# Performance work log

Measured on AMD Instinct MI355X. Metric: run time of the kernel, lower is better.

## Reference

```python
import jax, jax.numpy as jnp
import numpy as np
from jax import lax

B, S, D, H, O = 128, 256, 128, 512, 25
TEMP = 0.1


def _init(key, shape, scale):
    return jax.random.uniform(key, shape, jnp.float32, -scale, scale)


def setup_inputs() -> dict:
    key = jax.random.key(0)
    ks = jax.random.split(key, 24)
    sH = 1.0 / np.sqrt(H)
    s2H = 1.0 / np.sqrt(2 * H)
    sD = 1.0 / np.sqrt(D)
    inp = {
        "x": jax.random.normal(ks[0], (B, S, D), jnp.float32),
        "noise_u": jnp.clip(jax.random.uniform(ks[1], (S, B, 1), jnp.float32), 1e-6, 1 - 1e-6),
        # layer_cin: Linear(D, H)
        "w_cin": _init(ks[2], (D, H), sD), "b_cin": _init(ks[3], (H,), sD),
        # layer_c MLP: 2H->2H (x3, ReLU) -> 1
        "w1": _init(ks[4], (2 * H, 2 * H), s2H), "b1": _init(ks[5], (2 * H,), s2H),
        "w2": _init(ks[6], (2 * H, 2 * H), s2H), "b2": _init(ks[7], (2 * H,), s2H),
        "w3": _init(ks[8], (2 * H, 2 * H), s2H), "b3": _init(ks[9], (2 * H,), s2H),
        "w4": _init(ks[10], (2 * H, 1), s2H), "b4": _init(ks[11], (1,), s2H),
        # GRUCell(H, H): gates ordered (r, z, n)
        "w_ih": _init(ks[12], (H, 3 * H), sH), "b_ih": _init(ks[13], (3 * H,), sH),
        "w_hh": _init(ks[14], (H, 3 * H), sH), "b_hh": _init(ks[15], (3 * H,), sH),
        # output Linear(H, O)
        "w_out": _init(ks[16], (H, O), sH), "b_out": _init(ks[17], (O,), sH),
    }
    return inp


def _gru_cell(x, h, w_ih, b_ih, w_hh, b_hh):
    gx = x @ w_ih + b_ih  # [B, 3H]
    gh = h @ w_hh + b_hh
    xr, xz, xn = jnp.split(gx, 3, axis=-1)
    hr, hz, hn = jnp.split(gh, 3, axis=-1)
    r = jax.nn.sigmoid(xr + hr)
    z = jax.nn.sigmoid(xz + hz)
    n = jnp.tanh(xn + r * hn)
    return (1.0 - z) * n + z * h


def reference(x, noise_u, w_cin, b_cin, w1, b1, w2, b2, w3, b3, w4, b4,
              w_ih, b_ih, w_hh, b_hh, w_out, b_out):
    xs = jnp.transpose(x, (1, 0, 2))  # [S, B, D]

    def step(carry, inp):
        c, h, n = carry
        x_t, u = inp
        c_in = jnp.tanh(x_t @ w_cin + b_cin)  # [B, H]
        com = jnp.concatenate([c, c_in], axis=1)  # [B, 2H]
        z = jax.nn.relu(com @ w1 + b1)
        z = jax.nn.relu(z @ w2 + b2)
        z = jax.nn.relu(z @ w3 + b3)
        alpha_logit = z @ w4 + b4  # [B, 1]
        # RelaxedBernoulli(temp=0.1).sample(): sigmoid((logits + logistic noise)/T), detached
        logistic = jnp.log(u) - jnp.log1p(-u)
        alpha = lax.stop_gradient(jax.nn.sigmoid((alpha_logit + logistic) / TEMP))
        h_gru = _gru_cell(c, h, w_ih, b_ih, w_hh, b_hh)
        h_new = h * (1.0 - alpha) + alpha * h_gru
        new_n = n * (1.0 - alpha) + 1.0
        c_new = (c * n * (1.0 - alpha) + c_in) / new_n
        return (c_new, h_new, new_n), None

    c0 = jnp.zeros((B, H), x.dtype)
    h0 = jnp.zeros((B, H), x.dtype)
    n0 = jnp.zeros((B, 1), x.dtype)
    (c, h, n), _ = lax.scan(step, (c0, h0, n0), (xs, noise_u))
    h = _gru_cell(c, h, w_ih, b_ih, w_hh, b_hh)  # final post-loop GRU step
    return h @ w_out + b_out
```

## Files before the change

### kernel.cpp

```cpp
#include <hip/hip_runtime.h>
#include <math.h>

#define SLEN 256
#define BSZ  128
#define DIN  128
#define HSZ  512
#define HH2  1024
#define GG3  1536
#define OSZ  25

typedef _Float16 h8 __attribute__((ext_vector_type(8)));
typedef float    f4 __attribute__((ext_vector_type(4)));

struct P_t {
  const float *x, *noise, *b_cin, *b1, *b2, *b3, *w4, *b4, *b_ih, *b_hh, *w_out, *b_out;
  _Float16 *WT1, *WT2, *WT3, *WTih, *WThh, *WTcin;
  _Float16 *FW1, *FW2, *FW3, *FWih, *FWhh;
  _Float16 *CIN, *COMlo, *Z1, *Z2, *HF16;
  float *LOGI, *GX, *GH, *PART, *HF32, *CF32, *NF32;
  float *out;
};

__device__ __forceinline__ f4 mfma16(h8 a, h8 b, f4 c) {
  return __builtin_amdgcn_mfma_f32_16x16x32_f16(a, b, c, 0, 0, 0);
}

__global__ __launch_bounds__(256) void transpose_cvt(const float* __restrict__ src,
    _Float16* __restrict__ dst, int K, int N) {
  __shared__ float tl[32][33];
  int nt = N >> 5;
  int bx = blockIdx.x % nt, by = blockIdx.x / nt;
  int n0 = bx << 5, k0 = by << 5;
  int tx = threadIdx.x & 31, ty = threadIdx.x >> 5;
#pragma unroll
  for (int i = 0; i < 4; ++i) {
    int r = ty + (i << 3);
    tl[r][tx] = src[(size_t)(k0 + r) * N + n0 + tx];
  }
  __syncthreads();
#pragma unroll
  for (int i = 0; i < 4; ++i) {
    int r = ty + (i << 3);
    dst[(size_t)(n0 + r) * K + k0 + tx] = (_Float16)tl[tx][r];
  }
}

__global__ __launch_bounds__(512) void fragpack(const _Float16* __restrict__ src,
    _Float16* __restrict__ dst, int K) {
  int ct = blockIdx.x;
  int chunks = (K / 32) * 64;
  for (int idx = threadIdx.x; idx < chunks; idx += 512) {
    int i = idx >> 6, lane = idx & 63;
    int mlw = lane & 15, qw = lane >> 4;
    *(h8*)(dst + ((size_t)ct * (K / 32) + i) * 512 + (size_t)lane * 8) =
        *(const h8*)(src + ((size_t)ct * 16 + mlw) * K + i * 32 + qw * 8);
  }
}

__global__ __launch_bounds__(256) void cin_kernel(P_t P) {
  int tid = blockIdx.x * blockDim.x + threadIdx.x;
  if (tid < SLEN * BSZ) {
    float u = P.noise[tid];
    P.LOGI[tid] = logf(u) - log1pf(-u);
  }
  int gw = tid >> 6, lane = tid & 63;
  int nw = (gridDim.x * blockDim.x) >> 6;
  int ml = lane & 15, q = lane >> 4;
  const int MT = (SLEN * BSZ) / 16;
  for (int tt = gw; tt < MT * 8; tt += nw) {
    int mt = tt & (MT - 1), nt = tt / MT;
    int m0 = mt * 16, n0 = nt * 64;
    int m = m0 + ml, b = m & 127, s = m >> 7;
    const float* ap = P.x + ((size_t)b * SLEN + s) * DIN + q * 8;
    const _Float16* bp = P.WTcin + (size_t)(n0 + ml) * DIN + q * 8;
    f4 a0 = {0,0,0,0}, a1 = a0, a2 = a0, a3 = a0;
#pragma unroll
    for (int k = 0; k < DIN; k += 32) {
      f4 lo = *(const f4*)(ap + k);
      f4 hi = *(const f4*)(ap + k + 4);
      h8 av;
      av[0] = (_Float16)lo[0]; av[1] = (_Float16)lo[1];
      av[2] = (_Float16)lo[2]; av[3] = (_Float16)lo[3];
      av[4] = (_Float16)hi[0]; av[5] = (_Float16)hi[1];
      av[6] = (_Float16)hi[2]; av[7] = (_Float16)hi[3];
      a0 = mfma16(av, *(const h8*)(bp + k),            a0);
      a1 = mfma16(av, *(const h8*)(bp + 16*DIN + k),   a1);
      a2 = mfma16(av, *(const h8*)(bp + 32*DIN + k),   a2);
      a3 = mfma16(av, *(const h8*)(bp + 48*DIN + k),   a3);
    }
#pragma unroll
    for (int r = 0; r < 4; ++r) {
      int row = m0 + q * 4 + r;
      int c0 = n0 + ml;
      P.CIN[(size_t)row * HSZ + c0     ] = (_Float16)tanhf(a0[r] + P.b_cin[c0]);
      P.CIN[(size_t)row * HSZ + c0 + 16] = (_Float16)tanhf(a1[r] + P.b_cin[c0 + 16]);
      P.CIN[(size_t)row * HSZ + c0 + 32] = (_Float16)tanhf(a2[r] + P.b_cin[c0 + 32]);
      P.CIN[(size_t)row * HSZ + c0 + 48] = (_Float16)tanhf(a3[r] + P.b_cin[c0 + 48]);
    }
  }
}

__global__ __launch_bounds__(256) void init_kernel(P_t P) {
  int idx = blockIdx.x * 256 + threadIdx.x;
  if (idx < BSZ * HSZ) {
    P.HF32[idx] = 0.f; P.CF32[idx] = 0.f;
    P.HF16[idx] = (_Float16)0.f; P.COMlo[idx] = (_Float16)0.f;
  }
  if (idx < BSZ) P.NF32[idx] = 0.f;
}

__global__ __launch_bounds__(256) void step_a(P_t P, int t, int base) {
  const int tid = threadIdx.x;
  const int lane = tid & 63, wv = tid >> 6;
  const int ml = lane & 15, q = lane >> 4;
  const int g = base + blockIdx.x * 4 + wv;
  f4 acc = {0.f, 0.f, 0.f, 0.f};
  if (g < 512) {
    int rt = g & 7, ct = g >> 3;
    int m0 = rt * 16, col = ct * 16 + ml;
    const _Float16* a0 = P.COMlo + (size_t)(m0 + ml) * HSZ + q * 8;
    const _Float16* a1 = P.CIN + ((size_t)t * BSZ + m0 + ml) * HSZ + q * 8;
    const _Float16* bp = P.FW1 + (size_t)ct * 32 * 512 + (size_t)lane * 8;
#pragma unroll
    for (int i = 0; i < 16; ++i)
      acc = mfma16(*(const h8*)(a0 + i * 32), *(const h8*)(bp + (size_t)i * 512), acc);
#pragma unroll
    for (int i = 0; i < 16; ++i)
      acc = mfma16(*(const h8*)(a1 + i * 32), *(const h8*)(bp + (size_t)(16 + i) * 512), acc);
    float bia = P.b1[col];
#pragma unroll
    for (int j = 0; j < 4; ++j)
      P.Z1[(size_t)(m0 + q * 4 + j) * HH2 + col] = (_Float16)fmaxf(acc[j] + bia, 0.f);
  } else if (g < 1280) {
    int u = g - 512, rt = u & 7, ct = u >> 3;
    int m0 = rt * 16, col = ct * 16 + ml;
    const _Float16* a0 = P.COMlo + (size_t)(m0 + ml) * HSZ + q * 8;
    const _Float16* bp = P.FWih + (size_t)ct * 16 * 512 + (size_t)lane * 8;
#pragma unroll
    for (int i = 0; i < 16; ++i)
      acc = mfma16(*(const h8*)(a0 + i * 32), *(const h8*)(bp + (size_t)i * 512), acc);
    float bia = P.b_ih[col];
#pragma unroll
    for (int j = 0; j < 4; ++j)
      P.GX[(size_t)(m0 + q * 4 + j) * GG3 + col] = acc[j] + bia;
  } else {
    int u = g - 1280, rt = u & 7, ct = u >> 3;
    int m0 = rt * 16, col = ct * 16 + ml;
    const _Float16* a0 = P.HF16 + (size_t)(m0 + ml) * HSZ + q * 8;
    const _Float16* bp = P.FWhh + (size_t)ct * 16 * 512 + (size_t)lane * 8;
#pragma unroll
    for (int i = 0; i < 16; ++i)
      acc = mfma16(*(const h8*)(a0 + i * 32), *(const h8*)(bp + (size_t)i * 512), acc);
    float bia = P.b_hh[col];
#pragma unroll
    for (int j = 0; j < 4; ++j)
      P.GH[(size_t)(m0 + q * 4 + j) * GG3 + col] = acc[j] + bia;
  }
}

__global__ __launch_bounds__(256) void step_b(P_t P) {
  const int tid = threadIdx.x;
  const int lane = tid & 63, wv = tid >> 6;
  const int ml = lane & 15, q = lane >> 4;
  const int g = blockIdx.x * 4 + wv;
  int rt = g & 7, ct = g >> 3;
  int m0 = rt * 16, col = ct * 16 + ml;
  const _Float16* a0 = P.Z1 + (size_t)(m0 + ml) * HH2 + q * 8;
  const _Float16* bp = P.FW2 + (size_t)ct * 32 * 512 + (size_t)lane * 8;
  f4 acc = {0.f, 0.f, 0.f, 0.f};
#pragma unroll
  for (int i = 0; i < 32; ++i)
    acc = mfma16(*(const h8*)(a0 + i * 32), *(const h8*)(bp + (size_t)i * 512), acc);
  float bia = P.b2[col];
#pragma unroll
  for (int j = 0; j < 4; ++j)
    P.Z2[(size_t)(m0 + q * 4 + j) * HH2 + col] = (_Float16)fmaxf(acc[j] + bia, 0.f);
}

__global__ __launch_bounds__(256) void step_c(P_t P) {
  const int tid = threadIdx.x;
  const int lane = tid & 63, wv = tid >> 6;
  const int ml = lane & 15, q = lane >> 4;
  const int g = blockIdx.x * 4 + wv;
  int rt = g & 7, ct = g >> 3;
  int m0 = rt * 16, col = ct * 16 + ml;
  const _Float16* a0 = P.Z2 + (size_t)(m0 + ml) * HH2 + q * 8;
  const _Float16* bp = P.FW3 + (size_t)ct * 32 * 512 + (size_t)lane * 8;
  f4 acc = {0.f, 0.f, 0.f, 0.f};
#pragma unroll
  for (int i = 0; i < 32; ++i)
    acc = mfma16(*(const h8*)(a0 + i * 32), *(const h8*)(bp + (size_t)i * 512), acc);
  float bia = P.b3[col], w4v = P.w4[col];
#pragma unroll
  for (int j = 0; j < 4; ++j) {
    float v = fmaxf(acc[j] + bia, 0.f) * w4v;
    v += __shfl_xor(v, 1); v += __shfl_xor(v, 2);
    v += __shfl_xor(v, 4); v += __shfl_xor(v, 8);
    if (ml == 0) P.PART[(size_t)ct * BSZ + m0 + q * 4 + j] = v;
  }
}

__global__ __launch_bounds__(512) void step_d(P_t P, int t) {
  __shared__ float sa[4];
  const int r = blockIdx.x, tid = threadIdx.x;
  if (tid < 64) {
    float v = P.PART[(size_t)tid * BSZ + r];
#pragma unroll
    for (int off = 32; off > 0; off >>= 1) v += __shfl_xor(v, off);
    if (tid == 0) {
      float lg = (v + P.b4[0] + P.LOGI[(size_t)t * BSZ + r]) * 10.0f;
      float alpha = 1.f / (1.f + expf(-lg));
      float om = 1.f - alpha;
      float n_old = P.NF32[r];
      float nnew = n_old * om + 1.f;
      P.NF32[r] = nnew;
      sa[0] = alpha; sa[1] = om; sa[2] = n_old * om; sa[3] = nnew;
    }
  }
  __syncthreads();
  float alpha = sa[0], om = sa[1], nom = sa[2], nnew = sa[3];
  int col = tid;
  size_t go = (size_t)r * GG3 + col;
  float xr = P.GX[go], xz = P.GX[go + 512], xn = P.GX[go + 1024];
  float hr = P.GH[go], hz = P.GH[go + 512], hn = P.GH[go + 1024];
  float rg = 1.f / (1.f + expf(-(xr + hr)));
  float zg = 1.f / (1.f + expf(-(xz + hz)));
  float ng = tanhf(xn + rg * hn);
  size_t ho = (size_t)r * HSZ + col;
  float h_old = P.HF32[ho];
  float hg = (1.f - zg) * ng + zg * h_old;
  float hnew = h_old * om + alpha * hg;
  P.HF32[ho] = hnew; P.HF16[ho] = (_Float16)hnew;
  float c_old = P.CF32[ho];
  float cin_t = (float)P.CIN[((size_t)t * BSZ + r) * HSZ + col];
  float cnew = (c_old * nom + cin_t) / nnew;
  P.CF32[ho] = cnew; P.COMlo[ho] = (_Float16)cnew;
}

__global__ __launch_bounds__(512) void final_kernel(P_t P) {
  __shared__ float hf[512];
  const int r = blockIdx.x, tid = threadIdx.x;
  const int lane = tid & 63, wv = tid >> 6;
  {
    int col = tid;
    size_t go = (size_t)r * GG3 + col;
    float xr = P.GX[go], xz = P.GX[go + 512], xn = P.GX[go + 1024];
    float hr = P.GH[go], hz = P.GH[go + 512], hn = P.GH[go + 1024];
    float rg = 1.f / (1.f + expf(-(xr + hr)));
    float zg = 1.f / (1.f + expf(-(xz + hz)));
    float ng = tanhf(xn + rg * hn);
    float h_old = P.HF32[(size_t)r * HSZ + col];
    hf[col] = (1.f - zg) * ng + zg * h_old;
  }
  __syncthreads();
  for (int c = wv; c < OSZ; c += 8) {
    float v = 0.f;
#pragma unroll
    for (int j = 0; j < 8; ++j)
      v += hf[lane + 64 * j] * P.w_out[(size_t)(lane + 64 * j) * OSZ + c];
#pragma unroll
    for (int off = 32; off > 0; off >>= 1) v += __shfl_xor(v, off);
    if (lane == 0) P.out[r * OSZ + c] = v + P.b_out[c];
  }
}

extern "C" void kernel_launch(void* const* d_in, const int* in_sizes, int n_in,
                              void* d_out, int out_size, void* d_ws, size_t ws_size,
                              hipStream_t stream) {
  const float* x     = (const float*)d_in[0];
  const float* noise = (const float*)d_in[1];
  const float* w_cin = (const float*)d_in[2];
  const float* b_cin = (const float*)d_in[3];
  const float* w1    = (const float*)d_in[4];
  const float* b1    = (const float*)d_in[5];
  const float* w2    = (const float*)d_in[6];
  const float* b2    = (const float*)d_in[7];
  const float* w3    = (const float*)d_in[8];
  const float* b3    = (const float*)d_in[9];
  const float* w4    = (const float*)d_in[10];
  const float* b4    = (const float*)d_in[11];
  const float* w_ih  = (const float*)d_in[12];
  const float* b_ih  = (const float*)d_in[13];
  const float* w_hh  = (const float*)d_in[14];
  const float* b_hh  = (const float*)d_in[15];
  const float* w_out = (const float*)d_in[16];
  const float* b_out = (const float*)d_in[17];

  char* ws = (char*)d_ws;
  size_t off = 0;
  auto alloc = [&](size_t bytes) -> void* {
    void* p = ws + off;
    off = (off + bytes + 255) & ~(size_t)255;
    return p;
  };

  P_t P;
  P.x = x; P.noise = noise; P.b_cin = b_cin; P.b1 = b1; P.b2 = b2; P.b3 = b3;
  P.w4 = w4; P.b4 = b4; P.b_ih = b_ih; P.b_hh = b_hh; P.w_out = w_out; P.b_out = b_out;
  P.WT1   = (_Float16*)alloc((size_t)HH2 * HH2 * 2);
  P.WT2   = (_Float16*)alloc((size_t)HH2 * HH2 * 2);
  P.WT3   = (_Float16*)alloc((size_t)HH2 * HH2 * 2);
  P.WTih  = (_Float16*)alloc((size_t)GG3 * HSZ * 2);
  P.WThh  = (_Float16*)alloc((size_t)GG3 * HSZ * 2);
  P.WTcin = (_Float16*)alloc((size_t)HSZ * DIN * 2);
  P.FW1   = (_Float16*)alloc((size_t)HH2 * HH2 * 2);
  P.FW2   = (_Float16*)alloc((size_t)HH2 * HH2 * 2);
  P.FW3   = (_Float16*)alloc((size_t)HH2 * HH2 * 2);
  P.FWih  = (_Float16*)alloc((size_t)GG3 * HSZ * 2);
  P.FWhh  = (_Float16*)alloc((size_t)GG3 * HSZ * 2);
  P.CIN   = (_Float16*)alloc((size_t)SLEN * BSZ * HSZ * 2);
  P.COMlo = (_Float16*)alloc((size_t)BSZ * HSZ * 2);
  P.Z1    = (_Float16*)alloc((size_t)BSZ * HH2 * 2);
  P.Z2    = (_Float16*)alloc((size_t)BSZ * HH2 * 2);
  P.HF16  = (_Float16*)alloc((size_t)BSZ * HSZ * 2);
  P.LOGI  = (float*)alloc((size_t)SLEN * BSZ * 4);
  P.GX    = (float*)alloc((size_t)BSZ * GG3 * 4);
  P.GH    = (float*)alloc((size_t)BSZ * GG3 * 4);
  P.PART  = (float*)alloc((size_t)64 * BSZ * 4);
  P.HF32  = (float*)alloc((size_t)BSZ * HSZ * 4);
  P.CF32  = (float*)alloc((size_t)BSZ * HSZ * 4);
  P.NF32  = (float*)alloc((size_t)BSZ * 4);
  P.out   = (float*)d_out;

  transpose_cvt<<<(HH2/32)*(HH2/32), 256, 0, stream>>>(w1, P.WT1, HH2, HH2);
  transpose_cvt<<<(HH2/32)*(HH2/32), 256, 0, stream>>>(w2, P.WT2, HH2, HH2);
  transpose_cvt<<<(HH2/32)*(HH2/32), 256, 0, stream>>>(w3, P.WT3, HH2, HH2);
  transpose_cvt<<<(GG3/32)*(HSZ/32), 256, 0, stream>>>(w_ih, P.WTih, HSZ, GG3);
  transpose_cvt<<<(GG3/32)*(HSZ/32), 256, 0, stream>>>(w_hh, P.WThh, HSZ, GG3);
  transpose_cvt<<<(HSZ/32)*(DIN/32), 256, 0, stream>>>(w_cin, P.WTcin, DIN, HSZ);
  fragpack<<<HH2/16, 512, 0, stream>>>(P.WT1, P.FW1, HH2);
  fragpack<<<HH2/16, 512, 0, stream>>>(P.WT2, P.FW2, HH2);
  fragpack<<<HH2/16, 512, 0, stream>>>(P.WT3, P.FW3, HH2);
  fragpack<<<GG3/16, 512, 0, stream>>>(P.WTih, P.FWih, HSZ);
  fragpack<<<GG3/16, 512, 0, stream>>>(P.WThh, P.FWhh, HSZ);

  cin_kernel<<<1024, 256, 0, stream>>>(P);
  init_kernel<<<256, 256, 0, stream>>>(P);

  for (int t = 0; t < SLEN; ++t) {
    step_a<<<512, 256, 0, stream>>>(P, t, 0);
    step_b<<<128, 256, 0, stream>>>(P);
    step_c<<<128, 256, 0, stream>>>(P);
    step_d<<<BSZ, 512, 0, stream>>>(P, t);
  }
  step_a<<<384, 256, 0, stream>>>(P, 0, 512);
  final_kernel<<<BSZ, 512, 0, stream>>>(P);
}
```

Measured before the change: 7.152 ms.

## Fuse per-step state update into GEMM kernels, cutting launches per timestep

The separate step_d kernel goes away. The GRU gate math moves into the third MLP GEMM kernel, which writes HGRU, and the alpha/h/c/n update moves into the prologue of the first GEMM kernel. That kernel recomputes the update redundantly in each block and stages the fp16 c, h and c_in tiles in LDS. State is now double-buffered, and only one block per row tile writes the fp32 state back. This removes one kernel launch and its global round trip per timestep (256 in total), at the cost of redundant elementwise work in every k1 block and extra LDS traffic.

After: 7.037 ms. About the same (-1.6%).

```diff
diff --git a/kernel.cpp b/kernel.cpp
--- a/kernel.cpp
+++ b/kernel.cpp
@@ -10,14 +10,16 @@
 #define OSZ  25
 
 typedef _Float16 h8 __attribute__((ext_vector_type(8)));
+typedef _Float16 h4v __attribute__((ext_vector_type(4)));
 typedef float    f4 __attribute__((ext_vector_type(4)));
 
 struct P_t {
   const float *x, *noise, *b_cin, *b1, *b2, *b3, *w4, *b4, *b_ih, *b_hh, *w_out, *b_out;
   _Float16 *WT1, *WT2, *WT3, *WTih, *WThh, *WTcin;
   _Float16 *FW1, *FW2, *FW3, *FWih, *FWhh;
-  _Float16 *CIN, *COMlo, *Z1, *Z2, *HF16;
-  float *LOGI, *GX, *GH, *PART, *HF32, *CF32, *NF32;
+  _Float16 *CIN, *Z1, *Z2;
+  float *LOGI, *GX, *GH, *PART, *HGRU;
+  float *CF, *HF, *NF;
   float *out;
 };
 
@@ -102,55 +104,132 @@
 
 __global__ __launch_bounds__(256) void init_kernel(P_t P) {
   int idx = blockIdx.x * 256 + threadIdx.x;
-  if (idx < BSZ * HSZ) {
-    P.HF32[idx] = 0.f; P.CF32[idx] = 0.f;
-    P.HF16[idx] = (_Float16)0.f; P.COMlo[idx] = (_Float16)0.f;
-  }
-  if (idx < BSZ) P.NF32[idx] = 0.f;
-}
-
-__global__ __launch_bounds__(256) void step_a(P_t P, int t, int base) {
+  if (idx < 2 * BSZ * HSZ) { P.CF[idx] = 0.f; P.HF[idx] = 0.f; }
+  if (idx < 2 * BSZ) P.NF[idx] = 0.f;
+}
+
+__global__ __launch_bounds__(256) void step_k1(P_t P, int it) {
   const int tid = threadIdx.x;
   const int lane = tid & 63, wv = tid >> 6;
   const int ml = lane & 15, q = lane >> 4;
-  const int g = base + blockIdx.x * 4 + wv;
-  f4 acc = {0.f, 0.f, 0.f, 0.f};
-  if (g < 512) {
-    int rt = g & 7, ct = g >> 3;
-    int m0 = rt * 16, col = ct * 16 + ml;
-    const _Float16* a0 = P.COMlo + (size_t)(m0 + ml) * HSZ + q * 8;
-    const _Float16* a1 = P.CIN + ((size_t)t * BSZ + m0 + ml) * HSZ + q * 8;
-    const _Float16* bp = P.FW1 + (size_t)ct * 32 * 512 + (size_t)lane * 8;
-#pragma unroll
-    for (int i = 0; i < 16; ++i)
-      acc = mfma16(*(const h8*)(a0 + i * 32), *(const h8*)(bp + (size_t)i * 512), acc);
-#pragma unroll
-    for (int i = 0; i < 16; ++i)
-      acc = mfma16(*(const h8*)(a1 + i * 32), *(const h8*)(bp + (size_t)(16 + i) * 512), acc);
-    float bia = P.b1[col];
-#pragma unroll
-    for (int j = 0; j < 4; ++j)
-      P.Z1[(size_t)(m0 + q * 4 + j) * HH2 + col] = (_Float16)fmaxf(acc[j] + bia, 0.f);
-  } else if (g < 1280) {
-    int u = g - 512, rt = u & 7, ct = u >> 3;
-    int m0 = rt * 16, col = ct * 16 + ml;
-    const _Float16* a0 = P.COMlo + (size_t)(m0 + ml) * HSZ + q * 8;
+  const int b = blockIdx.x;
+  const int rt = b >> 6, bu = b & 63;
+  const int m0 = rt << 4;
+
+  __shared__ _Float16 sC[16][520];
+  __shared__ _Float16 sH[16][520];
+  __shared__ _Float16 sCIN[16][520];
+  __shared__ float sAl[16], sNOM[16], sNN[16];
+
+  if (it == 0) {
+    for (int c4 = tid; c4 < 2048; c4 += 256) {
+      int rl = c4 >> 7, cb = (c4 & 127) << 2;
+      h4v z = {(_Float16)0.f, (_Float16)0.f, (_Float16)0.f, (_Float16)0.f};
+      *(h4v*)&sC[rl][cb] = z;
+      *(h4v*)&sH[rl][cb] = z;
+    }
+  } else {
+    const int s = it - 1;
+    const float* CFo = P.CF + (size_t)((s + 1) & 1) * BSZ * HSZ;
+    const float* HFo = P.HF + (size_t)((s + 1) & 1) * BSZ * HSZ;
+    const float* NFo = P.NF + ((s + 1) & 1) * BSZ;
+    float* CFn = P.CF + (size_t)(s & 1) * BSZ * HSZ;
+    float* HFn = P.HF + (size_t)(s & 1) * BSZ * HSZ;
+    float* NFn = P.NF + (s & 1) * BSZ;
+    {
+      int rl = tid >> 4, sg = tid & 15;
+      int row = m0 + rl;
+      float v = P.PART[(size_t)(sg * 4 + 0) * BSZ + row]
+              + P.PART[(size_t)(sg * 4 + 1) * BSZ + row]
+              + P.PART[(size_t)(sg * 4 + 2) * BSZ + row]
+              + P.PART[(size_t)(sg * 4 + 3) * BSZ + row];
+      v += __shfl_xor(v, 1); v += __shfl_xor(v, 2);
+      v += __shfl_xor(v, 4); v += __shfl_xor(v, 8);
+      if (sg == 0) {
+        float lg = (v + P.b4[0] + P.LOGI[(size_t)s * BSZ + row]) * 10.0f;
+        float al = 1.f / (1.f + expf(-lg));
+        float om = 1.f - al;
+        float no = NFo[row];
+        float nn = no * om + 1.f;
+        sAl[rl] = al; sNOM[rl] = no * om; sNN[rl] = nn;
+        if (bu == 0) NFn[row] = nn;
+      }
+    }
+    __syncthreads();
+    for (int c4 = tid; c4 < 2048; c4 += 256) {
+      int rl = c4 >> 7, cb = (c4 & 127) << 2;
+      int row = m0 + rl;
+      size_t go = (size_t)row * HSZ + cb;
+      f4 hg = *(const f4*)(P.HGRU + go);
+      f4 ho = *(const f4*)(HFo + go);
+      f4 co = *(const f4*)(CFo + go);
+      h4v ci = *(const h4v*)(P.CIN + ((size_t)s * BSZ + row) * HSZ + cb);
+      float al = sAl[rl], om = 1.f - al, nom = sNOM[rl], nn = sNN[rl];
+      f4 hn, cn;
+#pragma unroll
+      for (int j = 0; j < 4; ++j) {
+        hn[j] = ho[j] * om + al * hg[j];
+        cn[j] = (co[j] * nom + (float)ci[j]) / nn;
+      }
+      h4v c16, h16;
+#pragma unroll
+      for (int j = 0; j < 4; ++j) { c16[j] = (_Float16)cn[j]; h16[j] = (_Float16)hn[j]; }
+      *(h4v*)&sC[rl][cb] = c16;
+      *(h4v*)&sH[rl][cb] = h16;
+      if (bu == 0) {
+        *(f4*)(CFn + go) = cn;
+        *(f4*)(HFn + go) = hn;
+      }
+    }
+  }
+  if (bu < 16 && it < SLEN) {
+    for (int c8 = tid; c8 < 1024; c8 += 256) {
+      int rl = c8 >> 6, cb = (c8 & 63) << 3;
+      *(h8*)&sCIN[rl][cb] =
+          *(const h8*)(P.CIN + ((size_t)it * BSZ + m0 + rl) * HSZ + cb);
+    }
+  }
+  __syncthreads();
+
+  const int u = bu * 4 + wv;
+  if (u < 64) {
+    if (it < SLEN) {
+      int ct = u, col = (ct << 4) + ml;
+      const _Float16* bp = P.FW1 + (size_t)ct * 32 * 512 + (size_t)lane * 8;
+      const _Float16* ac = &sC[ml][q * 8];
+      const _Float16* ai = &sCIN[ml][q * 8];
+      f4 acc = {0.f, 0.f, 0.f, 0.f};
+#pragma unroll
+      for (int k = 0; k < 16; ++k)
+        acc = mfma16(*(const h8*)(ac + k * 32), *(const h8*)(bp + (size_t)k * 512), acc);
+#pragma unroll
+      for (int k = 0; k < 16; ++k)
+        acc = mfma16(*(const h8*)(ai + k * 32), *(const h8*)(bp + (size_t)(16 + k) * 512), acc);
+      float bia = P.b1[col];
+#pragma unroll
+      for (int j = 0; j < 4; ++j)
+        P.Z1[(size_t)(m0 + q * 4 + j) * HH2 + col] = (_Float16)fmaxf(acc[j] + bia, 0.f);
+    }
+  } else if (u < 160) {
+    int ct = u - 64, col = (ct << 4) + ml;
     const _Float16* bp = P.FWih + (size_t)ct * 16 * 512 + (size_t)lane * 8;
-#pragma unroll
-    for (int i = 0; i < 16; ++i)
-      acc = mfma16(*(const h8*)(a0 + i * 32), *(const h8*)(bp + (size_t)i * 512), acc);
+    const _Float16* a0 = &sC[ml][q * 8];
+    f4 acc = {0.f, 0.f, 0.f, 0.f};
+#pragma unroll
+    for (int k = 0; k < 16; ++k)
+      acc = mfma16(*(const h8*)(a0 + k * 32), *(const h8*)(bp + (size_t)k * 512), acc);
     float bia = P.b_ih[col];
 #pragma unroll
     for (int j = 0; j < 4; ++j)
       P.GX[(size_t)(m0 + q * 4 + j) * GG3 + col] = acc[j] + bia;
   } else {
-    int u = g - 1280, rt = u & 7, ct = u >> 3;
-    int m0 = rt * 16, col = ct * 16 + ml;
-    const _Float16* a0 = P.HF16 + (size_t)(m0 + ml) * HSZ + q * 8;
+    int ct = u - 160, col = (ct << 4) + ml;
     const _Float16* bp = P.FWhh + (size_t)ct * 16 * 512 + (size_t)lane * 8;
-#pragma unroll
-    for (int i = 0; i < 16; ++i)
-      acc = mfma16(*(const h8*)(a0 + i * 32), *(const h8*)(bp + (size_t)i * 512), acc);
+    const _Float16* a0 = &sH[ml][q * 8];
+    f4 acc = {0.f, 0.f, 0.f, 0.f};
+#pragma unroll
+    for (int k = 0; k < 16; ++k)
+      acc = mfma16(*(const h8*)(a0 + k * 32), *(const h8*)(bp + (size_t)k * 512), acc);
     float bia = P.b_hh[col];
 #pragma unroll
     for (int j = 0; j < 4; ++j)
@@ -158,7 +237,7 @@
   }
 }
 
-__global__ __launch_bounds__(256) void step_b(P_t P) {
+__global__ __launch_bounds__(256) void step_k2(P_t P) {
   const int tid = threadIdx.x;
   const int lane = tid & 63, wv = tid >> 6;
   const int ml = lane & 15, q = lane >> 4;
@@ -177,70 +256,53 @@
     P.Z2[(size_t)(m0 + q * 4 + j) * HH2 + col] = (_Float16)fmaxf(acc[j] + bia, 0.f);
 }
 
-__global__ __launch_bounds__(256) void step_c(P_t P) {
+__global__ __launch_bounds__(256) void step_k3(P_t P, int it) {
   const int tid = threadIdx.x;
   const int lane = tid & 63, wv = tid >> 6;
   const int ml = lane & 15, q = lane >> 4;
   const int g = blockIdx.x * 4 + wv;
-  int rt = g & 7, ct = g >> 3;
-  int m0 = rt * 16, col = ct * 16 + ml;
-  const _Float16* a0 = P.Z2 + (size_t)(m0 + ml) * HH2 + q * 8;
-  const _Float16* bp = P.FW3 + (size_t)ct * 32 * 512 + (size_t)lane * 8;
-  f4 acc = {0.f, 0.f, 0.f, 0.f};
-#pragma unroll
-  for (int i = 0; i < 32; ++i)
-    acc = mfma16(*(const h8*)(a0 + i * 32), *(const h8*)(bp + (size_t)i * 512), acc);
-  float bia = P.b3[col], w4v = P.w4[col];
-#pragma unroll
-  for (int j = 0; j < 4; ++j) {
-    float v = fmaxf(acc[j] + bia, 0.f) * w4v;
-    v += __shfl_xor(v, 1); v += __shfl_xor(v, 2);
-    v += __shfl_xor(v, 4); v += __shfl_xor(v, 8);
-    if (ml == 0) P.PART[(size_t)ct * BSZ + m0 + q * 4 + j] = v;
-  }
-}
-
-__global__ __launch_bounds__(512) void step_d(P_t P, int t) {
-  __shared__ float sa[4];
-  const int r = blockIdx.x, tid = threadIdx.x;
-  if (tid < 64) {
-    float v = P.PART[(size_t)tid * BSZ + r];
-#pragma unroll
-    for (int off = 32; off > 0; off >>= 1) v += __shfl_xor(v, off);
-    if (tid == 0) {
-      float lg = (v + P.b4[0] + P.LOGI[(size_t)t * BSZ + r]) * 10.0f;
-      float alpha = 1.f / (1.f + expf(-lg));
-      float om = 1.f - alpha;
-      float n_old = P.NF32[r];
-      float nnew = n_old * om + 1.f;
-      P.NF32[r] = nnew;
-      sa[0] = alpha; sa[1] = om; sa[2] = n_old * om; sa[3] = nnew;
-    }
-  }
-  __syncthreads();
-  float alpha = sa[0], om = sa[1], nom = sa[2], nnew = sa[3];
-  int col = tid;
-  size_t go = (size_t)r * GG3 + col;
-  float xr = P.GX[go], xz = P.GX[go + 512], xn = P.GX[go + 1024];
-  float hr = P.GH[go], hz = P.GH[go + 512], hn = P.GH[go + 1024];
-  float rg = 1.f / (1.f + expf(-(xr + hr)));
-  float zg = 1.f / (1.f + expf(-(xz + hz)));
-  float ng = tanhf(xn + rg * hn);
-  size_t ho = (size_t)r * HSZ + col;
-  float h_old = P.HF32[ho];
-  float hg = (1.f - zg) * ng + zg * h_old;
-  float hnew = h_old * om + alpha * hg;
-  P.HF32[ho] = hnew; P.HF16[ho] = (_Float16)hnew;
-  float c_old = P.CF32[ho];
-  float cin_t = (float)P.CIN[((size_t)t * BSZ + r) * HSZ + col];
-  float cnew = (c_old * nom + cin_t) / nnew;
-  P.CF32[ho] = cnew; P.COMlo[ho] = (_Float16)cnew;
+  {
+    int rt = g & 7, ct = g >> 3;
+    int m0 = rt * 16, col = ct * 16 + ml;
+    const _Float16* a0 = P.Z2 + (size_t)(m0 + ml) * HH2 + q * 8;
+    const _Float16* bp = P.FW3 + (size_t)ct * 32 * 512 + (size_t)lane * 8;
+    f4 acc = {0.f, 0.f, 0.f, 0.f};
+#pragma unroll
+    for (int i = 0; i < 32; ++i)
+      acc = mfma16(*(const h8*)(a0 + i * 32), *(const h8*)(bp + (size_t)i * 512), acc);
+    float bia = P.b3[col], w4v = P.w4[col];
+#pragma unroll
+    for (int j = 0; j < 4; ++j) {
+      float v = fmaxf(acc[j] + bia, 0.f) * w4v;
+      v += __shfl_xor(v, 1); v += __shfl_xor(v, 2);
+      v += __shfl_xor(v, 4); v += __shfl_xor(v, 8);
+      if (ml == 0) P.PART[(size_t)ct * BSZ + m0 + q * 4 + j] = v;
+    }
+  }
+  {
+    const float* HFo = P.HF + (size_t)((it + 1) & 1) * BSZ * HSZ;
+    int e0 = blockIdx.x * 512;
+#pragma unroll
+    for (int ee = 0; ee < 2; ++ee) {
+      int e = e0 + tid + ee * 256;
+      int row = e >> 9, col = e & 511;
+      size_t g3 = (size_t)row * GG3 + col;
+      float xr = P.GX[g3], xz = P.GX[g3 + 512], xn = P.GX[g3 + 1024];
+      float hr = P.GH[g3], hz = P.GH[g3 + 512], hn = P.GH[g3 + 1024];
+      float rg = 1.f / (1.f + expf(-(xr + hr)));
+      float zg = 1.f / (1.f + expf(-(xz + hz)));
+      float ng = tanhf(xn + rg * hn);
+      float ho = HFo[(size_t)row * HSZ + col];
+      P.HGRU[(size_t)row * HSZ + col] = (1.f - zg) * ng + zg * ho;
+    }
+  }
 }
 
 __global__ __launch_bounds__(512) void final_kernel(P_t P) {
   __shared__ float hf[512];
   const int r = blockIdx.x, tid = threadIdx.x;
   const int lane = tid & 63, wv = tid >> 6;
+  const float* HFo = P.HF + (size_t)((SLEN - 1) & 1) * BSZ * HSZ;
   {
     int col = tid;
     size_t go = (size_t)r * GG3 + col;
@@ -249,7 +311,7 @@
     float rg = 1.f / (1.f + expf(-(xr + hr)));
     float zg = 1.f / (1.f + expf(-(xz + hz)));
     float ng = tanhf(xn + rg * hn);
-    float h_old = P.HF32[(size_t)r * HSZ + col];
+    float h_old = HFo[(size_t)r * HSZ + col];
     hf[col] = (1.f - zg) * ng + zg * h_old;
   }
   __syncthreads();
@@ -309,17 +371,16 @@
   P.FWih  = (_Float16*)alloc((size_t)GG3 * HSZ * 2);
   P.FWhh  = (_Float16*)alloc((size_t)GG3 * HSZ * 2);
   P.CIN   = (_Float16*)alloc((size_t)SLEN * BSZ * HSZ * 2);
-  P.COMlo = (_Float16*)alloc((size_t)BSZ * HSZ * 2);
   P.Z1    = (_Float16*)alloc((size_t)BSZ * HH2 * 2);
   P.Z2    = (_Float16*)alloc((size_t)BSZ * HH2 * 2);
-  P.HF16  = (_Float16*)alloc((size_t)BSZ * HSZ * 2);
   P.LOGI  = (float*)alloc((size_t)SLEN * BSZ * 4);
   P.GX    = (float*)alloc((size_t)BSZ * GG3 * 4);
   P.GH    = (float*)alloc((size_t)BSZ * GG3 * 4);
   P.PART  = (float*)alloc((size_t)64 * BSZ * 4);
-  P.HF32  = (float*)alloc((size_t)BSZ * HSZ * 4);
-  P.CF32  = (float*)alloc((size_t)BSZ * HSZ * 4);
-  P.NF32  = (float*)alloc((size_t)BSZ * 4);
+  P.HGRU  = (float*)alloc((size_t)BSZ * HSZ * 4);
+  P.CF    = (float*)alloc((size_t)2 * BSZ * HSZ * 4);
+  P.HF    = (float*)alloc((size_t)2 * BSZ * HSZ * 4);
+  P.NF    = (float*)alloc((size_t)2 * BSZ * 4);
   P.out   = (float*)d_out;
 
   transpose_cvt<<<(HH2/32)*(HH2/32), 256, 0, stream>>>(w1, P.WT1, HH2, HH2);
@@ -335,14 +396,13 @@
   fragpack<<<GG3/16, 512, 0, stream>>>(P.WThh, P.FWhh, HSZ);
 
   cin_kernel<<<1024, 256, 0, stream>>>(P);
-  init_kernel<<<256, 256, 0, stream>>>(P);
+  init_kernel<<<512, 256, 0, stream>>>(P);
 
   for (int t = 0; t < SLEN; ++t) {
-    step_a<<<512, 256, 0, stream>>>(P, t, 0);
-    step_b<<<128, 256, 0, stream>>>(P);
-    step_c<<<128, 256, 0, stream>>>(P);
-    step_d<<<BSZ, 512, 0, stream>>>(P, t);
-  }
-  step_a<<<384, 256, 0, stream>>>(P, 0, 512);
+    step_k1<<<512, 256, 0, stream>>>(P, t);
+    step_k2<<<128, 256, 0, stream>>>(P);
+    step_k3<<<128, 256, 0, stream>>>(P, t);
+  }
+  step_k1<<<512, 256, 0, stream>>>(P, SLEN);
   final_kernel<<<BSZ, 512, 0, stream>>>(P);
 }
```
